# Performance work log

Hardware: AMD Instinct MI355X
Metric: run time of the kernel (lower is better)

The kernel has to match this reference:

```python
import jax, jax.numpy as jnp
import numpy as np

T, B, INP, HID = 256, 128, 512, 512
LAST_K, RSIZE = 32, 64
ATTN = 1.0
NEG = -1e30  # stands in for float('-inf') in the mask; softmax weight is exactly 0 either way


def setup_inputs() -> dict:
    key = jax.random.key(0)
    ks = jax.random.split(key, 6)
    xav = lambda fi, fo: (2.0 / (fi + fo)) ** 0.5
    x = jax.random.normal(ks[0], (T, B, INP), jnp.float32)
    # torch Linear weights stored transposed so y = x @ W (+ b)
    Uw = jax.random.normal(ks[1], (INP, HID), jnp.float32) * xav(INP, HID)
    Ub = jnp.zeros((HID,), jnp.float32)
    Vw = jax.random.normal(ks[2], (HID, HID), jnp.float32) * xav(HID, HID)
    Uaw = jax.random.normal(ks[3], (HID, HID), jnp.float32) * xav(HID, HID)
    Vaw = jax.random.normal(ks[4], (HID, HID), jnp.float32) * xav(HID, HID)
    v = jax.random.normal(ks[5], (HID,), jnp.float32) * xav(1, HID)
    return {"x": x, "Uw": Uw, "Ub": Ub, "Vw": Vw, "Uaw": Uaw, "Vaw": Vaw, "v": v}


def reference(x, Uw, Ub, Vw, Uaw, Vaw, v):
    Tlen, Bsz, _ = x.shape
    H = Uw.shape[1]
    bidx = jnp.arange(Bsz)

    def step(carry, inp):
        xt, t = inp
        st, buf, slot_time, long_mem, long_mask, long_scores, buck, fcnt, lids = carry

        def first(_):
            # hidden is None -> zeros, so V(hidden) == 0; st is the pre-nonlinearity h
            pre = xt @ Uw + Ub
            return pre, jnp.tanh(pre), long_scores

        def later(_):
            va_st = st @ Vaw                                  # [B,H]
            # short-term memory attention (buf slot p holds h_{slot_time[p]}, -1 = empty)
            es = jnp.einsum('kbh,h->kb', jnp.tanh(va_st[None] + buf @ Uaw), v)
            es = jnp.where(slot_time[:, None] >= 0, es, NEG)  # mask empty slots
            es_l = jnp.einsum('rbh,h->rb', jnp.tanh(va_st[None] + long_mem @ Uaw), v) + long_mask
            alphas = jax.nn.softmax(jnp.concatenate([es, es_l], axis=0), axis=0)  # [K+R,B]
            comb = jnp.concatenate([buf, long_mem], axis=0)   # [K+R,B,H]
            ct = jnp.einsum('mb,mbh->bh', alphas, comb)
            last_h = buf[(t - 1) % LAST_K]                    # memory[-1] == h_{t-1}
            st_new = 0.5 * (last_h + ct * ATTN)
            h = jnp.tanh(xt @ Uw + Ub + st_new @ Vw)
            # detached accumulation of attention mass per timestep (long_scores[time] += alpha)
            det = jax.lax.stop_gradient(alphas[:LAST_K])
            valid = slot_time >= 0
            ls = long_scores.at[jnp.where(valid, slot_time, 0)].add(
                jnp.where(valid[:, None], det, 0.0))
            return st_new, h, ls

        st, h, long_scores = jax.lax.cond(t == 0, first, later, None)

        # --- conditional bucket eviction: candidate is h_{t-LAST_K} (oldest in buf) ---
        evict_step = t >= LAST_K
        cand = buf[t % LAST_K]                                # slot about to be overwritten
        score_t = long_scores[jnp.maximum(t - LAST_K, 0)]     # [B]
        minp = jnp.argmin(buck, axis=1)                       # [B]
        not_full = fcnt < RSIZE
        replace = score_t > buck[bidx, minp]
        do = evict_step & (not_full | replace)
        pos = jnp.where(not_full, fcnt, minp)                 # [B]
        long_mem = long_mem.at[pos, bidx].set(jnp.where(do[:, None], cand, long_mem[pos, bidx]))
        long_mask = long_mask.at[pos, bidx].set(jnp.where(do, 0.0, long_mask[pos, bidx]))
        buck = buck.at[bidx, pos].set(jnp.where(do, score_t, buck[bidx, pos]))
        lids = lids.at[bidx, pos].set(jnp.where(do, (t - LAST_K).astype(jnp.float32), lids[bidx, pos]))
        fcnt = jnp.where(do & not_full, fcnt + 1, fcnt)

        # append h to short-term circular buffer
        buf = buf.at[t % LAST_K].set(h)
        slot_time = slot_time.at[t % LAST_K].set(t)

        return (st, buf, slot_time, long_mem, long_mask, long_scores, buck, fcnt, lids), h

    carry0 = (
        jnp.zeros((Bsz, H), jnp.float32),                 # st
        jnp.zeros((LAST_K, Bsz, H), jnp.float32),         # short-term memory buffer
        -jnp.ones((LAST_K,), jnp.int32),                  # time stored in each buf slot
        jnp.zeros((RSIZE, Bsz, H), jnp.float32),          # long_mem buckets
        jnp.full((RSIZE, Bsz), NEG, jnp.float32),         # long_mask
        jnp.zeros((Tlen, Bsz), jnp.float32),              # long_scores
        jnp.zeros((Bsz, RSIZE), jnp.float32),             # buck_scores
        jnp.zeros((Bsz,), jnp.int32),                     # bucket fill count
        -jnp.ones((Bsz, RSIZE), jnp.float32),             # long_ids
    )
    _, hs = jax.lax.scan(step, carry0, (x, jnp.arange(Tlen)))
    return hs  # [T,B,H] hidden state at every step
```

## Files before the change

### kernel.cpp

```cpp
#include <hip/hip_runtime.h>
#include <hip/hip_bf16.h>
#include <cstddef>

#define kT 256
#define kB 128
#define kINP 512
#define kH 512
#define kK 32
#define kR 64
#define kNEG (-1e30f)

__device__ __forceinline__ void ag_store(float* p, float v) {
    __hip_atomic_store(p, v, __ATOMIC_RELAXED, __HIP_MEMORY_SCOPE_AGENT);
}
__device__ __forceinline__ float ag_load(const float* p) {
    return __hip_atomic_load(p, __ATOMIC_RELAXED, __HIP_MEMORY_SCOPE_AGENT);
}

__device__ __forceinline__ float ftanh(float x)
{
    float e = __expf(2.0f * x);
    return 1.0f - 2.0f * __builtin_amdgcn_rcpf(e + 1.0f);
}

__global__ __launch_bounds__(256) void gemm_xu(
    const float* __restrict__ A, const float* __restrict__ W,
    const float* __restrict__ bias, float* __restrict__ C)
{
    __shared__ float At[32][68];
    __shared__ float Ws[32][68];
    const int tid = threadIdx.x;
    const int n0 = blockIdx.x * 64;
    const int m0 = blockIdx.y * 64;
    const int tx = tid & 15, ty = tid >> 4;
    const int arow = tid >> 3, ak = (tid & 7) << 2;
    const int wrow = tid >> 4, wc = (tid & 15) << 2;

    float acc[4][4] = {};

    for (int k0 = 0; k0 < kINP; k0 += 32) {
        float4 a0 = *reinterpret_cast<const float4*>(&A[(size_t)(m0 + arow) * kINP + k0 + ak]);
        float4 a1 = *reinterpret_cast<const float4*>(&A[(size_t)(m0 + 32 + arow) * kINP + k0 + ak]);
        float4 w0 = *reinterpret_cast<const float4*>(&W[(size_t)(k0 + wrow) * kH + n0 + wc]);
        float4 w1 = *reinterpret_cast<const float4*>(&W[(size_t)(k0 + wrow + 16) * kH + n0 + wc]);
        __syncthreads();
        At[ak + 0][arow] = a0.x; At[ak + 1][arow] = a0.y;
        At[ak + 2][arow] = a0.z; At[ak + 3][arow] = a0.w;
        At[ak + 0][32 + arow] = a1.x; At[ak + 1][32 + arow] = a1.y;
        At[ak + 2][32 + arow] = a1.z; At[ak + 3][32 + arow] = a1.w;
        *reinterpret_cast<float4*>(&Ws[wrow][wc]) = w0;
        *reinterpret_cast<float4*>(&Ws[wrow + 16][wc]) = w1;
        __syncthreads();
#pragma unroll
        for (int kk = 0; kk < 32; ++kk) {
            float4 a4 = *reinterpret_cast<float4*>(&At[kk][ty * 4]);
            float4 w4 = *reinterpret_cast<float4*>(&Ws[kk][tx * 4]);
            float a_[4] = {a4.x, a4.y, a4.z, a4.w};
            float w_[4] = {w4.x, w4.y, w4.z, w4.w};
#pragma unroll
            for (int r = 0; r < 4; ++r)
#pragma unroll
                for (int c = 0; c < 4; ++c)
                    acc[r][c] += a_[r] * w_[c];
        }
    }

#pragma unroll
    for (int r = 0; r < 4; ++r) {
        int m = m0 + ty * 4 + r;
#pragma unroll
        for (int c = 0; c < 4; ++c) {
            int n = n0 + tx * 4 + c;
            C[(size_t)m * kH + n] = acc[r][c] + bias[n];
        }
    }
}

__global__ __launch_bounds__(256) void init_flags_k(int* __restrict__ flags)
{
    int i = blockIdx.x * 256 + threadIdx.x;
    if (i < kB * 3 * 2) flags[i] = 0;
}

__global__ __launch_bounds__(1024) void rnn_pair(
    const float* __restrict__ Vw, const float* __restrict__ Vaw,
    const float* __restrict__ Uaw, const float* __restrict__ vvec,
    const float* __restrict__ XU, float* __restrict__ lngU,
    float* __restrict__ hs, float* __restrict__ esx,
    float* __restrict__ stx, int* __restrict__ flags)
{
    extern __shared__ float dyn[];
    float* shortH = dyn;
    float* shortU = dyn + 32 * 256;
    float* longH  = dyn + 64 * 256;
    float* part   = dyn + 128 * 256;
    const int PSTR = 264;

    const int bid = blockIdx.x;
    const int b = bid >> 1, half = bid & 1;
    const int C0 = half << 8;
    const int P0 = (half ^ 1) << 8;
    const int tid = threadIdx.x;
    const int kq = tid >> 6;
    const int lane = tid & 63;
    const int c4 = lane << 2;

    __shared__ __align__(16) float h_sh[512];
    __shared__ __align__(16) float st_sh[512];
    __shared__ __align__(16) float va_sh[256];
    __shared__ __align__(16) float v_sh[256];
    __shared__ float es_own[96], es_sh[96], w_sh[96];
    __shared__ int   rowm[96];
    __shared__ float lsc_sh[kT];
    __shared__ float buck_sh[kR];
    __shared__ int   lidx_sh[kR];
    __shared__ int   fcnt_sh, evict_pos;
    __shared__ float red0, red1;

    float* lngU_b = lngU + (size_t)bid * kR * 256;

    int* fC_own = &flags[(b * 3 + 0) * 2 + half];
    int* fB_own = &flags[(b * 3 + 1) * 2 + half];
    int* fS_own = &flags[(b * 3 + 2) * 2 + half];
    int* fC_par = &flags[(b * 3 + 0) * 2 + (half ^ 1)];
    int* fB_par = &flags[(b * 3 + 1) * 2 + (half ^ 1)];
    int* fS_par = &flags[(b * 3 + 2) * 2 + (half ^ 1)];

    auto wait_ge = [&](int* f, int target) {
        if (tid == 0) {
            while (__hip_atomic_load(f, __ATOMIC_RELAXED, __HIP_MEMORY_SCOPE_AGENT) < target)
                __builtin_amdgcn_s_sleep(1);
        }
        __syncthreads();
    };
    auto set_flag = [&](int* f, int val) {
        __syncthreads();
        if (tid == 0)
            __hip_atomic_store(f, val, __ATOMIC_RELAXED, __HIP_MEMORY_SCOPE_AGENT);
    };

    if (tid < 256) { v_sh[tid] = vvec[C0 + tid]; lsc_sh[tid] = 0.0f; }
    if (tid < kR) { buck_sh[tid] = 0.0f; lidx_sh[tid] = -1; }
    if (tid == 0) fcnt_sh = 0;
    if (tid < 512) st_sh[tid] = XU[(size_t)b * kH + tid];
    __syncthreads();
    if (tid < 256) {
        float h0 = tanhf(st_sh[C0 + tid]);
        h_sh[C0 + tid] = h0;
        shortH[tid] = h0;
        ag_store(&hs[(size_t)b * kH + C0 + tid], h0);
    }
    set_flag(fC_own, 1);
    {
        float4 acc = {0, 0, 0, 0};
#pragma unroll 8
        for (int k = kq; k < kH; k += 16) {
            float s = st_sh[k];
            const float4 w = *reinterpret_cast<const float4*>(&Vaw[(size_t)k * kH + C0 + c4]);
            acc.x += s * w.x; acc.y += s * w.y; acc.z += s * w.z; acc.w += s * w.w;
        }
        *reinterpret_cast<float4*>(&part[kq * PSTR + c4]) = acc;
        __syncthreads();
        if (tid < 256) {
            float s = 0.0f;
#pragma unroll
            for (int j = 0; j < 16; ++j) s += part[j * PSTR + tid];
            va_sh[tid] = s;
        }
        __syncthreads();
    }

    for (int t = 1; t < kT; ++t) {
        float xu_reg = 0.0f;
        if (tid < 256) xu_reg = XU[((size_t)t * kB + b) * kH + C0 + tid];

        float4 accA = {0, 0, 0, 0};
#pragma unroll 8
        for (int k = C0 + kq; k < C0 + 256; k += 16) {
            float s = h_sh[k];
            const float4 w = *reinterpret_cast<const float4*>(&Uaw[(size_t)k * kH + C0 + c4]);
            accA.x += s * w.x; accA.y += s * w.y; accA.z += s * w.z; accA.w += s * w.w;
        }
        if (tid < 96) {
            int row;
            if (tid < kK) { int md = (t + 31 - tid) & 31; row = t - 1 - md; }
            else row = lidx_sh[tid - kK];
            rowm[tid] = row;
        }
        wait_ge(fC_par, t);
        if (tid < 256) h_sh[P0 + tid] = ag_load(&hs[((size_t)(t - 1) * kB + b) * kH + P0 + tid]);
        __syncthreads();
#pragma unroll 8
        for (int k = P0 + kq; k < P0 + 256; k += 16) {
            float s = h_sh[k];
            const float4 w = *reinterpret_cast<const float4*>(&Uaw[(size_t)k * kH + C0 + c4]);
            accA.x += s * w.x; accA.y += s * w.y; accA.z += s * w.z; accA.w += s * w.w;
        }
        *reinterpret_cast<float4*>(&part[kq * PSTR + c4]) = accA;
        __syncthreads();
        if (tid < 256) {
            float u = 0.0f;
#pragma unroll
            for (int j = 0; j < 16; ++j) u += part[j * PSTR + tid];
            shortU[((t - 1) & 31) * 256 + tid] = u;
        }
        __syncthreads();

        {
            float4 uu[6];
            int rv[6];
#pragma unroll
            for (int r = 0; r < 6; ++r) {
                int m = kq + (r << 4);
                int row = rowm[m];
                rv[r] = row;
                uu[r] = make_float4(0.f, 0.f, 0.f, 0.f);
                if (row >= 0) {
                    const float* up = (m < kK) ? &shortU[m * 256]
                                               : &lngU_b[(size_t)(m - kK) * 256];
                    uu[r] = *reinterpret_cast<const float4*>(&up[c4]);
                }
            }
            const float4 vav = *reinterpret_cast<const float4*>(&va_sh[c4]);
            const float4 vvv = *reinterpret_cast<const float4*>(&v_sh[c4]);
#pragma unroll
            for (int r = 0; r < 6; ++r) {
                float p = 0.0f;
                if (rv[r] >= 0) {
                    p = vvv.x * ftanh(vav.x + uu[r].x) + vvv.y * ftanh(vav.y + uu[r].y)
                      + vvv.z * ftanh(vav.z + uu[r].z) + vvv.w * ftanh(vav.w + uu[r].w);
                }
#pragma unroll
                for (int off = 32; off; off >>= 1) p += __shfl_down(p, off);
                if (lane == 0) es_own[kq + (r << 4)] = p;
            }
        }
        __syncthreads();
        if (tid < 96) ag_store(&esx[((size_t)b * 2 + half) * 96 + tid], es_own[tid]);
        set_flag(fB_own, t);
        wait_ge(fB_par, t);
        if (tid < 96) {
            float e = kNEG;
            if (rowm[tid] >= 0)
                e = es_own[tid] + ag_load(&esx[((size_t)b * 2 + (half ^ 1)) * 96 + tid]);
            es_sh[tid] = e;
        }
        __syncthreads();

        if (tid < 64) {
            float a = es_sh[tid];
            float c = (tid < 32) ? es_sh[64 + tid] : kNEG;
            float mx = fmaxf(a, c);
#pragma unroll
            for (int off = 32; off; off >>= 1) mx = fmaxf(mx, __shfl_xor(mx, off));
            if (tid == 0) red0 = mx;
        }
        __syncthreads();
        if (tid < 96) w_sh[tid] = __expf(es_sh[tid] - red0);
        __syncthreads();
        if (tid < 64) {
            float a = w_sh[tid] + ((tid < 32) ? w_sh[64 + tid] : 0.0f);
#pragma unroll
            for (int off = 32; off; off >>= 1) a += __shfl_xor(a, off);
            if (tid == 0) red1 = 1.0f / a;
        }
        __syncthreads();

        {
            float4 hv[6]; float wq[6];
#pragma unroll
            for (int r = 0; r < 6; ++r) {
                int m = kq + (r << 4);
                int row = rowm[m];
                hv[r] = make_float4(0.f, 0.f, 0.f, 0.f); wq[r] = 0.0f;
                if (row >= 0) {
                    const float* hp = (m < kK) ? &shortH[m * 256]
                                               : &longH[(m - kK) * 256];
                    hv[r] = *reinterpret_cast<const float4*>(&hp[c4]);
                    wq[r] = w_sh[m];
                }
            }
            float4 acc = {0, 0, 0, 0};
#pragma unroll
            for (int r = 0; r < 6; ++r) {
                acc.x += wq[r] * hv[r].x; acc.y += wq[r] * hv[r].y;
                acc.z += wq[r] * hv[r].z; acc.w += wq[r] * hv[r].w;
            }
            *reinterpret_cast<float4*>(&part[kq * PSTR + c4]) = acc;
        }
        __syncthreads();
        if (tid < 256) {
            float ct = 0.0f;
#pragma unroll
            for (int j = 0; j < 16; ++j) ct += part[j * PSTR + tid];
            float stv = 0.5f * (h_sh[C0 + tid] + ct * red1);
            st_sh[C0 + tid] = stv;
            ag_store(&stx[(size_t)b * kH + C0 + tid], stv);
        }
        set_flag(fS_own, t);

        if (tid < kK) {
            int row = rowm[tid];
            if (row >= 0) lsc_sh[row] += w_sh[tid] * red1;
        }
        __syncthreads();
        if (tid == 0) {
            int ep = -1;
            if (t >= kK) {
                float score = lsc_sh[t - kK];
                int fc = fcnt_sh;
                bool nf = fc < kR;
                float mn = buck_sh[0]; int mp = 0;
                for (int r = 1; r < kR; ++r) {
                    float bv = buck_sh[r];
                    if (bv < mn) { mn = bv; mp = r; }
                }
                if (nf || score > mn) {
                    ep = nf ? fc : mp;
                    lidx_sh[ep] = t - kK;
                    buck_sh[ep] = score;
                    if (nf) fcnt_sh = fc + 1;
                }
            }
            evict_pos = ep;
        }
        __syncthreads();
        if (evict_pos >= 0 && tid < 256) {
            longH[evict_pos * 256 + tid] = shortH[(t & 31) * 256 + tid];
            lngU_b[(size_t)evict_pos * 256 + tid] = shortU[(t & 31) * 256 + tid];
        }

        {
            float4 aw = {0, 0, 0, 0};
#pragma unroll 8
            for (int k = C0 + kq; k < C0 + 256; k += 16) {
                float s = st_sh[k];
                const float4 w = *reinterpret_cast<const float4*>(&Vw[(size_t)k * kH + C0 + c4]);
                aw.x += s * w.x; aw.y += s * w.y; aw.z += s * w.z; aw.w += s * w.w;
            }
            wait_ge(fS_par, t);
            if (tid < 256) st_sh[P0 + tid] = ag_load(&stx[(size_t)b * kH + P0 + tid]);
            __syncthreads();
#pragma unroll 8
            for (int k = P0 + kq; k < P0 + 256; k += 16) {
                float s = st_sh[k];
                const float4 w = *reinterpret_cast<const float4*>(&Vw[(size_t)k * kH + C0 + c4]);
                aw.x += s * w.x; aw.y += s * w.y; aw.z += s * w.z; aw.w += s * w.w;
            }
            *reinterpret_cast<float4*>(&part[kq * PSTR + c4]) = aw;
        }
        __syncthreads();
        if (tid < 256) {
            float hpre = xu_reg;
#pragma unroll
            for (int j = 0; j < 16; ++j) hpre += part[j * PSTR + tid];
            float hv = tanhf(hpre);
            h_sh[C0 + tid] = hv;
            shortH[(t & 31) * 256 + tid] = hv;
            ag_store(&hs[((size_t)t * kB + b) * kH + C0 + tid], hv);
        }
        set_flag(fC_own, t + 1);

        {
            float4 av = {0, 0, 0, 0};
#pragma unroll 8
            for (int k = kq; k < kH; k += 16) {
                float s = st_sh[k];
                const float4 w = *reinterpret_cast<const float4*>(&Vaw[(size_t)k * kH + C0 + c4]);
                av.x += s * w.x; av.y += s * w.y; av.z += s * w.z; av.w += s * w.w;
            }
            *reinterpret_cast<float4*>(&part[kq * PSTR + c4]) = av;
        }
        __syncthreads();
        if (tid < 256) {
            float vn = 0.0f;
#pragma unroll
            for (int j = 0; j < 16; ++j) vn += part[j * PSTR + tid];
            va_sh[tid] = vn;
        }
        __syncthreads();
    }
}

extern "C" void kernel_launch(void* const* d_in, const int* in_sizes, int n_in,
                              void* d_out, int out_size, void* d_ws, size_t ws_size,
                              hipStream_t stream)
{
    const float* x   = (const float*)d_in[0];
    const float* Uw  = (const float*)d_in[1];
    const float* Ub  = (const float*)d_in[2];
    const float* Vw  = (const float*)d_in[3];
    const float* Uaw = (const float*)d_in[4];
    const float* Vaw = (const float*)d_in[5];
    const float* vv  = (const float*)d_in[6];
    float* hs = (float*)d_out;

    float* ws = (float*)d_ws;
    const size_t TBH = (size_t)kT * kB * kH;
    float* XU   = ws;
    float* lngU = XU + TBH;
    float* esx  = lngU + (size_t)2 * kB * kR * 256;
    float* stx  = esx + (size_t)kB * 2 * 96;
    int*   flags = (int*)(stx + (size_t)kB * kH);

    const int dyn_bytes = (32 * 256 + 32 * 256 + 64 * 256 + 16 * 264) * 4;
    hipFuncSetAttribute(reinterpret_cast<const void*>(rnn_pair),
                        hipFuncAttributeMaxDynamicSharedMemorySize, dyn_bytes);

    init_flags_k<<<3, 256, 0, stream>>>(flags);

    gemm_xu<<<dim3(kH / 64, (kT * kB) / 64), 256, 0, stream>>>(x, Uw, Ub, XU);

    rnn_pair<<<2 * kB, 1024, dyn_bytes, stream>>>(
        Vw, Vaw, Uaw, vv, XU, lngU, hs, esx, stx, flags);
}
```

Baseline: 5.658 ms.

## Overlap Vaw projection with Uaw matvec by splitting waves across both

Instead of computing st@Vaw as a separate phase at the end of each step (and once before the loop), half of the waves now compute it while the other half compute the own-half h@Uaw product. The remote-half Uaw product after the parity wait is handled by those same 8 waves only. Both reductions run in one pass, dropping two barriers per step and putting the Vaw work in the window before the cross-block flag wait. The risk is that the post-wait Uaw work now uses half as many waves, which lengthens that stage of the critical path.

```diff
diff --git a/kernel.cpp b/kernel.cpp
--- a/kernel.cpp
+++ b/kernel.cpp
@@ -102,6 +102,7 @@
     const int P0 = (half ^ 1) << 8;
     const int tid = threadIdx.x;
     const int kq = tid >> 6;
+    const int kq8 = kq & 7;
     const int lane = tid & 63;
     const int c4 = lane << 2;
 
@@ -151,35 +152,26 @@
         ag_store(&hs[(size_t)b * kH + C0 + tid], h0);
     }
     set_flag(fC_own, 1);
-    {
-        float4 acc = {0, 0, 0, 0};
-#pragma unroll 8
-        for (int k = kq; k < kH; k += 16) {
-            float s = st_sh[k];
-            const float4 w = *reinterpret_cast<const float4*>(&Vaw[(size_t)k * kH + C0 + c4]);
-            acc.x += s * w.x; acc.y += s * w.y; acc.z += s * w.z; acc.w += s * w.w;
-        }
-        *reinterpret_cast<float4*>(&part[kq * PSTR + c4]) = acc;
-        __syncthreads();
-        if (tid < 256) {
-            float s = 0.0f;
-#pragma unroll
-            for (int j = 0; j < 16; ++j) s += part[j * PSTR + tid];
-            va_sh[tid] = s;
-        }
-        __syncthreads();
-    }
 
     for (int t = 1; t < kT; ++t) {
         float xu_reg = 0.0f;
         if (tid < 256) xu_reg = XU[((size_t)t * kB + b) * kH + C0 + tid];
 
         float4 accA = {0, 0, 0, 0};
-#pragma unroll 8
-        for (int k = C0 + kq; k < C0 + 256; k += 16) {
-            float s = h_sh[k];
-            const float4 w = *reinterpret_cast<const float4*>(&Uaw[(size_t)k * kH + C0 + c4]);
-            accA.x += s * w.x; accA.y += s * w.y; accA.z += s * w.z; accA.w += s * w.w;
+        if (kq >= 8) {
+#pragma unroll 8
+            for (int k = kq8; k < kH; k += 8) {
+                float s = st_sh[k];
+                const float4 w = *reinterpret_cast<const float4*>(&Vaw[(size_t)k * kH + C0 + c4]);
+                accA.x += s * w.x; accA.y += s * w.y; accA.z += s * w.z; accA.w += s * w.w;
+            }
+        } else {
+#pragma unroll 8
+            for (int k = C0 + kq8; k < C0 + 256; k += 8) {
+                float s = h_sh[k];
+                const float4 w = *reinterpret_cast<const float4*>(&Uaw[(size_t)k * kH + C0 + c4]);
+                accA.x += s * w.x; accA.y += s * w.y; accA.z += s * w.z; accA.w += s * w.w;
+            }
         }
         if (tid < 96) {
             int row;
@@ -190,19 +182,28 @@
         wait_ge(fC_par, t);
         if (tid < 256) h_sh[P0 + tid] = ag_load(&hs[((size_t)(t - 1) * kB + b) * kH + P0 + tid]);
         __syncthreads();
-#pragma unroll 8
-        for (int k = P0 + kq; k < P0 + 256; k += 16) {
-            float s = h_sh[k];
-            const float4 w = *reinterpret_cast<const float4*>(&Uaw[(size_t)k * kH + C0 + c4]);
-            accA.x += s * w.x; accA.y += s * w.y; accA.z += s * w.z; accA.w += s * w.w;
+        if (kq < 8) {
+#pragma unroll 8
+            for (int k = P0 + kq8; k < P0 + 256; k += 8) {
+                float s = h_sh[k];
+                const float4 w = *reinterpret_cast<const float4*>(&Uaw[(size_t)k * kH + C0 + c4]);
+                accA.x += s * w.x; accA.y += s * w.y; accA.z += s * w.z; accA.w += s * w.w;
+            }
         }
         *reinterpret_cast<float4*>(&part[kq * PSTR + c4]) = accA;
         __syncthreads();
-        if (tid < 256) {
-            float u = 0.0f;
-#pragma unroll
-            for (int j = 0; j < 16; ++j) u += part[j * PSTR + tid];
-            shortU[((t - 1) & 31) * 256 + tid] = u;
+        if (tid < 512) {
+            int col = tid & 255;
+            float acc = 0.0f;
+            if (tid < 256) {
+#pragma unroll
+                for (int j = 0; j < 8; ++j) acc += part[j * PSTR + col];
+                shortU[((t - 1) & 31) * 256 + col] = acc;
+            } else {
+#pragma unroll
+                for (int j = 8; j < 16; ++j) acc += part[j * PSTR + col];
+                va_sh[col] = acc;
+            }
         }
         __syncthreads();
 
@@ -360,25 +361,6 @@
             ag_store(&hs[((size_t)t * kB + b) * kH + C0 + tid], hv);
         }
         set_flag(fC_own, t + 1);
-
-        {
-            float4 av = {0, 0, 0, 0};
-#pragma unroll 8
-            for (int k = kq; k < kH; k += 16) {
-                float s = st_sh[k];
-                const float4 w = *reinterpret_cast<const float4*>(&Vaw[(size_t)k * kH + C0 + c4]);
-                av.x += s * w.x; av.y += s * w.y; av.z += s * w.z; av.w += s * w.w;
-            }
-            *reinterpret_cast<float4*>(&part[kq * PSTR + c4]) = av;
-        }
-        __syncthreads();
-        if (tid < 256) {
-            float vn = 0.0f;
-#pragma unroll
-            for (int j = 0; j < 16; ++j) vn += part[j * PSTR + tid];
-            va_sh[tid] = vn;
-        }
-        __syncthreads();
     }
 }
 
```

Result: slower. 7.650 ms (+35.2%).

## Split recurrent kernel into quad blocks handling two batch rows per column quarter

Applied to the files above, without the earlier changes.

The per-step recurrence moves from a pair of blocks per batch row (each owning half the hidden columns) to groups of four blocks that each own a quarter of the columns for two batch rows. Each loaded weight float4 is reused across both batch rows, halving weight traffic per row, and each block's shared-memory footprint per row shrinks. In exchange, every step now needs four-way flag synchronization and gathers partial energies from three peers, which adds cross-block latency on the serial critical path. It also changes the lsc bookkeeping to a 64-entry ring that is reset after use.

```diff
diff --git a/kernel.cpp b/kernel.cpp
--- a/kernel.cpp
+++ b/kernel.cpp
@@ -79,10 +79,26 @@
 __global__ __launch_bounds__(256) void init_flags_k(int* __restrict__ flags)
 {
     int i = blockIdx.x * 256 + threadIdx.x;
-    if (i < kB * 3 * 2) flags[i] = 0;
-}
-
-__global__ __launch_bounds__(1024) void rnn_pair(
+    if (i < 64 * 3 * 4) flags[i] = 0;
+}
+
+#define MV_STEP(Wmat, xs, i, A0, A1) { \
+    int k_ = (i)*32 + (w << 1) + half32; \
+    const float4 wt_ = *reinterpret_cast<const float4*>(&Wmat[(size_t)k_ * kH + C0 + c4]); \
+    float s0_ = xs[0][k_], s1_ = xs[1][k_]; \
+    A0.x += s0_*wt_.x; A0.y += s0_*wt_.y; A0.z += s0_*wt_.z; A0.w += s0_*wt_.w; \
+    A1.x += s1_*wt_.x; A1.y += s1_*wt_.y; A1.z += s1_*wt_.z; A1.w += s1_*wt_.w; }
+
+#define MV_FINISH(A0, A1) { \
+    A0.x += __shfl_xor(A0.x, 32); A0.y += __shfl_xor(A0.y, 32); \
+    A0.z += __shfl_xor(A0.z, 32); A0.w += __shfl_xor(A0.w, 32); \
+    A1.x += __shfl_xor(A1.x, 32); A1.y += __shfl_xor(A1.y, 32); \
+    A1.z += __shfl_xor(A1.z, 32); A1.w += __shfl_xor(A1.w, 32); \
+    if (lane < 32) { \
+        *reinterpret_cast<float4*>(&part[(w*2 + 0)*128 + c4]) = A0; \
+        *reinterpret_cast<float4*>(&part[(w*2 + 1)*128 + c4]) = A1; } }
+
+__global__ __launch_bounds__(1024) void rnn_quad(
     const float* __restrict__ Vw, const float* __restrict__ Vaw,
     const float* __restrict__ Uaw, const float* __restrict__ vvec,
     const float* __restrict__ XU, float* __restrict__ lngU,
@@ -91,294 +107,304 @@
 {
     extern __shared__ float dyn[];
     float* shortH = dyn;
-    float* shortU = dyn + 32 * 256;
-    float* longH  = dyn + 64 * 256;
-    float* part   = dyn + 128 * 256;
-    const int PSTR = 264;
+    float* shortU = dyn + 8192;
+    float* longH  = dyn + 16384;
+    float* part   = dyn + 32768;
 
     const int bid = blockIdx.x;
-    const int b = bid >> 1, half = bid & 1;
-    const int C0 = half << 8;
-    const int P0 = (half ^ 1) << 8;
+    const int g = bid >> 2, q = bid & 3;
+    const int bA = g << 1;
+    const int C0 = q << 7;
     const int tid = threadIdx.x;
-    const int kq = tid >> 6;
+    const int w = tid >> 6;
     const int lane = tid & 63;
-    const int c4 = lane << 2;
-
-    __shared__ __align__(16) float h_sh[512];
-    __shared__ __align__(16) float st_sh[512];
-    __shared__ __align__(16) float va_sh[256];
-    __shared__ __align__(16) float v_sh[256];
-    __shared__ float es_own[96], es_sh[96], w_sh[96];
-    __shared__ int   rowm[96];
-    __shared__ float lsc_sh[kT];
-    __shared__ float buck_sh[kR];
-    __shared__ int   lidx_sh[kR];
-    __shared__ int   fcnt_sh, evict_pos;
-    __shared__ float red0, red1;
-
-    float* lngU_b = lngU + (size_t)bid * kR * 256;
-
-    int* fC_own = &flags[(b * 3 + 0) * 2 + half];
-    int* fB_own = &flags[(b * 3 + 1) * 2 + half];
-    int* fS_own = &flags[(b * 3 + 2) * 2 + half];
-    int* fC_par = &flags[(b * 3 + 0) * 2 + (half ^ 1)];
-    int* fB_par = &flags[(b * 3 + 1) * 2 + (half ^ 1)];
-    int* fS_par = &flags[(b * 3 + 2) * 2 + (half ^ 1)];
-
-    auto wait_ge = [&](int* f, int target) {
-        if (tid == 0) {
+    const int half32 = lane >> 5;
+    const int c4 = (lane & 31) << 2;
+    const int c2 = lane << 1;
+    const int i0 = q << 2;
+
+    __shared__ __align__(16) float h_sh[2][512];
+    __shared__ __align__(16) float st_sh[2][512];
+    __shared__ __align__(16) float va_sh[2][128];
+    __shared__ __align__(16) float v_sh[128];
+    __shared__ float es_own[2][96], es_sh[2][96], w_sh[2][96];
+    __shared__ int   rowm[2][96];
+    __shared__ float lsc_sh[2][64];
+    __shared__ float buck_sh[2][64];
+    __shared__ int   lidx_sh[2][64];
+    __shared__ int   fcnt_sh[2], evict_pos[2];
+    __shared__ float red0[2], red1[2];
+
+    float* lngU_b = lngU + (size_t)bid * 2 * kR * 128;
+    const int fbase = g * 12;
+
+    auto wait3 = [&](int phase, int target) {
+        if (tid < 3) {
+            int p = tid + (tid >= q ? 1 : 0);
+            int* f = &flags[fbase + phase * 4 + p];
             while (__hip_atomic_load(f, __ATOMIC_RELAXED, __HIP_MEMORY_SCOPE_AGENT) < target)
                 __builtin_amdgcn_s_sleep(1);
         }
         __syncthreads();
     };
-    auto set_flag = [&](int* f, int val) {
+    auto set_flag = [&](int phase, int val) {
         __syncthreads();
         if (tid == 0)
-            __hip_atomic_store(f, val, __ATOMIC_RELAXED, __HIP_MEMORY_SCOPE_AGENT);
+            __hip_atomic_store(&flags[fbase + phase * 4 + q], val,
+                               __ATOMIC_RELAXED, __HIP_MEMORY_SCOPE_AGENT);
     };
 
-    if (tid < 256) { v_sh[tid] = vvec[C0 + tid]; lsc_sh[tid] = 0.0f; }
-    if (tid < kR) { buck_sh[tid] = 0.0f; lidx_sh[tid] = -1; }
-    if (tid == 0) fcnt_sh = 0;
-    if (tid < 512) st_sh[tid] = XU[(size_t)b * kH + tid];
+    if (tid < 128) v_sh[tid] = vvec[C0 + tid];
+    if (tid < 128) {
+        int bb = tid >> 6, s = tid & 63;
+        lsc_sh[bb][s] = 0.0f; buck_sh[bb][s] = 0.0f; lidx_sh[bb][s] = -1;
+    }
+    if (tid < 2) fcnt_sh[tid] = 0;
+    {
+        int bb = tid >> 9, col = tid & 511;
+        st_sh[bb][col] = XU[(size_t)(bA + bb) * kH + col];
+    }
     __syncthreads();
     if (tid < 256) {
-        float h0 = tanhf(st_sh[C0 + tid]);
-        h_sh[C0 + tid] = h0;
-        shortH[tid] = h0;
-        ag_store(&hs[(size_t)b * kH + C0 + tid], h0);
-    }
-    set_flag(fC_own, 1);
+        int bb = tid >> 7, col = tid & 127;
+        float h0 = tanhf(st_sh[bb][C0 + col]);
+        h_sh[bb][C0 + col] = h0;
+        shortH[(bb * 32 + 0) * 128 + col] = h0;
+        ag_store(&hs[(size_t)(bA + bb) * kH + C0 + col], h0);
+    }
+    set_flag(0, 1);
     {
-        float4 acc = {0, 0, 0, 0};
-#pragma unroll 8
-        for (int k = kq; k < kH; k += 16) {
-            float s = st_sh[k];
-            const float4 w = *reinterpret_cast<const float4*>(&Vaw[(size_t)k * kH + C0 + c4]);
-            acc.x += s * w.x; acc.y += s * w.y; acc.z += s * w.z; acc.w += s * w.w;
-        }
-        *reinterpret_cast<float4*>(&part[kq * PSTR + c4]) = acc;
+        float4 a0 = {0,0,0,0}, a1 = {0,0,0,0};
+#pragma unroll
+        for (int i = 0; i < 16; ++i) MV_STEP(Vaw, st_sh, i, a0, a1);
+        MV_FINISH(a0, a1);
         __syncthreads();
         if (tid < 256) {
+            int bb = tid >> 7, col = tid & 127;
             float s = 0.0f;
 #pragma unroll
-            for (int j = 0; j < 16; ++j) s += part[j * PSTR + tid];
-            va_sh[tid] = s;
+            for (int j = 0; j < 16; ++j) s += part[(j * 2 + bb) * 128 + col];
+            va_sh[bb][col] = s;
         }
         __syncthreads();
     }
 
     for (int t = 1; t < kT; ++t) {
         float xu_reg = 0.0f;
-        if (tid < 256) xu_reg = XU[((size_t)t * kB + b) * kH + C0 + tid];
-
-        float4 accA = {0, 0, 0, 0};
-#pragma unroll 8
-        for (int k = C0 + kq; k < C0 + 256; k += 16) {
-            float s = h_sh[k];
-            const float4 w = *reinterpret_cast<const float4*>(&Uaw[(size_t)k * kH + C0 + c4]);
-            accA.x += s * w.x; accA.y += s * w.y; accA.z += s * w.z; accA.w += s * w.w;
-        }
-        if (tid < 96) {
+        if (tid < 256) {
+            int bb = tid >> 7, col = tid & 127;
+            xu_reg = XU[((size_t)t * kB + (bA + bb)) * kH + C0 + col];
+        }
+
+        float4 aU0 = {0,0,0,0}, aU1 = {0,0,0,0};
+#pragma unroll
+        for (int i = 0; i < 4; ++i) MV_STEP(Uaw, h_sh, i0 + i, aU0, aU1);
+        if (tid < 192) {
+            int bb = (tid >= 96), m = tid - bb * 96;
             int row;
-            if (tid < kK) { int md = (t + 31 - tid) & 31; row = t - 1 - md; }
-            else row = lidx_sh[tid - kK];
-            rowm[tid] = row;
-        }
-        wait_ge(fC_par, t);
-        if (tid < 256) h_sh[P0 + tid] = ag_load(&hs[((size_t)(t - 1) * kB + b) * kH + P0 + tid]);
-        __syncthreads();
-#pragma unroll 8
-        for (int k = P0 + kq; k < P0 + 256; k += 16) {
-            float s = h_sh[k];
-            const float4 w = *reinterpret_cast<const float4*>(&Uaw[(size_t)k * kH + C0 + c4]);
-            accA.x += s * w.x; accA.y += s * w.y; accA.z += s * w.z; accA.w += s * w.w;
-        }
-        *reinterpret_cast<float4*>(&part[kq * PSTR + c4]) = accA;
+            if (m < kK) { int md = (t + 31 - m) & 31; row = t - 1 - md; }
+            else row = lidx_sh[bb][m - kK];
+            rowm[bb][m] = row;
+        }
+        wait3(0, t);
+        if (tid < 768) {
+            int bb = tid / 384, j = tid - bb * 384;
+            int pq = j >> 7, col = j & 127;
+            int qq = pq + (pq >= q ? 1 : 0);
+            h_sh[bb][qq * 128 + col] =
+                ag_load(&hs[((size_t)(t - 1) * kB + (bA + bb)) * kH + qq * 128 + col]);
+        }
+        __syncthreads();
+        for (int i = 0; i < i0; ++i) MV_STEP(Uaw, h_sh, i, aU0, aU1);
+        for (int i = i0 + 4; i < 16; ++i) MV_STEP(Uaw, h_sh, i, aU0, aU1);
+        MV_FINISH(aU0, aU1);
         __syncthreads();
         if (tid < 256) {
+            int bb = tid >> 7, col = tid & 127;
             float u = 0.0f;
 #pragma unroll
-            for (int j = 0; j < 16; ++j) u += part[j * PSTR + tid];
-            shortU[((t - 1) & 31) * 256 + tid] = u;
+            for (int j = 0; j < 16; ++j) u += part[(j * 2 + bb) * 128 + col];
+            shortU[(bb * 32 + ((t - 1) & 31)) * 128 + col] = u;
         }
         __syncthreads();
 
         {
-            float4 uu[6];
-            int rv[6];
-#pragma unroll
-            for (int r = 0; r < 6; ++r) {
-                int m = kq + (r << 4);
-                int row = rowm[m];
-                rv[r] = row;
-                uu[r] = make_float4(0.f, 0.f, 0.f, 0.f);
+            int bb = w >> 3, wr = w & 7;
+            float2 vav = *reinterpret_cast<const float2*>(&va_sh[bb][c2]);
+            float2 vvv = *reinterpret_cast<const float2*>(&v_sh[c2]);
+#pragma unroll
+            for (int r = 0; r < 12; ++r) {
+                int m = wr + (r << 3);
+                int row = rowm[bb][m];
+                float p = 0.0f;
                 if (row >= 0) {
-                    const float* up = (m < kK) ? &shortU[m * 256]
-                                               : &lngU_b[(size_t)(m - kK) * 256];
-                    uu[r] = *reinterpret_cast<const float4*>(&up[c4]);
+                    const float* up = (m < kK) ? &shortU[(bb * 32 + m) * 128]
+                                               : &lngU_b[(size_t)(bb * kR + (m - kK)) * 128];
+                    float2 uu = *reinterpret_cast<const float2*>(&up[c2]);
+                    p = vvv.x * ftanh(vav.x + uu.x) + vvv.y * ftanh(vav.y + uu.y);
                 }
-            }
-            const float4 vav = *reinterpret_cast<const float4*>(&va_sh[c4]);
-            const float4 vvv = *reinterpret_cast<const float4*>(&v_sh[c4]);
-#pragma unroll
-            for (int r = 0; r < 6; ++r) {
-                float p = 0.0f;
-                if (rv[r] >= 0) {
-                    p = vvv.x * ftanh(vav.x + uu[r].x) + vvv.y * ftanh(vav.y + uu[r].y)
-                      + vvv.z * ftanh(vav.z + uu[r].z) + vvv.w * ftanh(vav.w + uu[r].w);
+#pragma unroll
+                for (int off = 32; off; off >>= 1) p += __shfl_down(p, off);
+                if (lane == 0) es_own[bb][m] = p;
+            }
+        }
+        __syncthreads();
+        if (tid < 192) {
+            int bb = (tid >= 96), m = tid - bb * 96;
+            ag_store(&esx[(size_t)bid * 192 + bb * 96 + m], es_own[bb][m]);
+        }
+        set_flag(1, t);
+        wait3(1, t);
+        if (tid < 192) {
+            int bb = (tid >= 96), m = tid - bb * 96;
+            float e = kNEG;
+            if (rowm[bb][m] >= 0) {
+                e = 0.0f;
+#pragma unroll
+                for (int p = 0; p < 4; ++p)
+                    e += ag_load(&esx[(size_t)(g * 4 + p) * 192 + bb * 96 + m]);
+            }
+            es_sh[bb][m] = e;
+        }
+        __syncthreads();
+
+        if (w < 2) {
+            float a = es_sh[w][lane];
+            float b2 = (lane < 32) ? es_sh[w][64 + lane] : kNEG;
+            float mx = fmaxf(a, b2);
+#pragma unroll
+            for (int off = 32; off; off >>= 1) mx = fmaxf(mx, __shfl_xor(mx, off));
+            if (lane == 0) red0[w] = mx;
+        }
+        __syncthreads();
+        if (tid < 192) {
+            int bb = (tid >= 96), m = tid - bb * 96;
+            w_sh[bb][m] = __expf(es_sh[bb][m] - red0[bb]);
+        }
+        __syncthreads();
+        if (w < 2) {
+            float a = w_sh[w][lane] + ((lane < 32) ? w_sh[w][64 + lane] : 0.0f);
+#pragma unroll
+            for (int off = 32; off; off >>= 1) a += __shfl_xor(a, off);
+            if (lane == 0) red1[w] = 1.0f / a;
+        }
+        __syncthreads();
+
+        {
+            int bb = w >> 3, wr = w & 7;
+            float2 acc = {0.0f, 0.0f};
+#pragma unroll
+            for (int r = 0; r < 12; ++r) {
+                int m = wr + (r << 3);
+                int row = rowm[bb][m];
+                if (row >= 0) {
+                    const float* hp = (m < kK) ? &shortH[(bb * 32 + m) * 128]
+                                               : &longH[(bb * kR + (m - kK)) * 128];
+                    float2 hv = *reinterpret_cast<const float2*>(&hp[c2]);
+                    float wq = w_sh[bb][m];
+                    acc.x += wq * hv.x; acc.y += wq * hv.y;
                 }
-#pragma unroll
-                for (int off = 32; off; off >>= 1) p += __shfl_down(p, off);
-                if (lane == 0) es_own[kq + (r << 4)] = p;
-            }
-        }
-        __syncthreads();
-        if (tid < 96) ag_store(&esx[((size_t)b * 2 + half) * 96 + tid], es_own[tid]);
-        set_flag(fB_own, t);
-        wait_ge(fB_par, t);
-        if (tid < 96) {
-            float e = kNEG;
-            if (rowm[tid] >= 0)
-                e = es_own[tid] + ag_load(&esx[((size_t)b * 2 + (half ^ 1)) * 96 + tid]);
-            es_sh[tid] = e;
-        }
-        __syncthreads();
+            }
+            *reinterpret_cast<float2*>(&part[w * 128 + c2]) = acc;
+        }
+        __syncthreads();
+        if (tid < 256) {
+            int bb = tid >> 7, col = tid & 127;
+            float ct = 0.0f;
+#pragma unroll
+            for (int j = 0; j < 8; ++j) ct += part[(bb * 8 + j) * 128 + col];
+            float stv = 0.5f * (h_sh[bb][C0 + col] + ct * red1[bb]);
+            st_sh[bb][C0 + col] = stv;
+            ag_store(&stx[(size_t)(bA + bb) * kH + C0 + col], stv);
+        }
+        set_flag(2, t);
 
         if (tid < 64) {
-            float a = es_sh[tid];
-            float c = (tid < 32) ? es_sh[64 + tid] : kNEG;
-            float mx = fmaxf(a, c);
-#pragma unroll
-            for (int off = 32; off; off >>= 1) mx = fmaxf(mx, __shfl_xor(mx, off));
-            if (tid == 0) red0 = mx;
-        }
-        __syncthreads();
-        if (tid < 96) w_sh[tid] = __expf(es_sh[tid] - red0);
-        __syncthreads();
-        if (tid < 64) {
-            float a = w_sh[tid] + ((tid < 32) ? w_sh[64 + tid] : 0.0f);
-#pragma unroll
-            for (int off = 32; off; off >>= 1) a += __shfl_xor(a, off);
-            if (tid == 0) red1 = 1.0f / a;
-        }
-        __syncthreads();
-
-        {
-            float4 hv[6]; float wq[6];
-#pragma unroll
-            for (int r = 0; r < 6; ++r) {
-                int m = kq + (r << 4);
-                int row = rowm[m];
-                hv[r] = make_float4(0.f, 0.f, 0.f, 0.f); wq[r] = 0.0f;
-                if (row >= 0) {
-                    const float* hp = (m < kK) ? &shortH[m * 256]
-                                               : &longH[(m - kK) * 256];
-                    hv[r] = *reinterpret_cast<const float4*>(&hp[c4]);
-                    wq[r] = w_sh[m];
-                }
-            }
-            float4 acc = {0, 0, 0, 0};
-#pragma unroll
-            for (int r = 0; r < 6; ++r) {
-                acc.x += wq[r] * hv[r].x; acc.y += wq[r] * hv[r].y;
-                acc.z += wq[r] * hv[r].z; acc.w += wq[r] * hv[r].w;
-            }
-            *reinterpret_cast<float4*>(&part[kq * PSTR + c4]) = acc;
-        }
-        __syncthreads();
-        if (tid < 256) {
-            float ct = 0.0f;
-#pragma unroll
-            for (int j = 0; j < 16; ++j) ct += part[j * PSTR + tid];
-            float stv = 0.5f * (h_sh[C0 + tid] + ct * red1);
-            st_sh[C0 + tid] = stv;
-            ag_store(&stx[(size_t)b * kH + C0 + tid], stv);
-        }
-        set_flag(fS_own, t);
-
-        if (tid < kK) {
-            int row = rowm[tid];
-            if (row >= 0) lsc_sh[row] += w_sh[tid] * red1;
-        }
-        __syncthreads();
-        if (tid == 0) {
-            int ep = -1;
+            int bb = tid >> 5, s = tid & 31;
+            int row = rowm[bb][s];
+            if (row >= 0) lsc_sh[bb][row & 63] += w_sh[bb][s] * red1[bb];
+        }
+        __syncthreads();
+        if (tid < 2) {
+            int bb = tid, ep = -1;
             if (t >= kK) {
-                float score = lsc_sh[t - kK];
-                int fc = fcnt_sh;
+                float score = lsc_sh[bb][(t - kK) & 63];
+                lsc_sh[bb][(t - kK) & 63] = 0.0f;
+                int fc = fcnt_sh[bb];
                 bool nf = fc < kR;
-                float mn = buck_sh[0]; int mp = 0;
-                for (int r = 1; r < kR; ++r) {
-                    float bv = buck_sh[r];
-                    if (bv < mn) { mn = bv; mp = r; }
+                float mn = buck_sh[bb][0]; int mp = 0;
+                for (int r2 = 1; r2 < kR; ++r2) {
+                    float bv = buck_sh[bb][r2];
+                    if (bv < mn) { mn = bv; mp = r2; }
                 }
                 if (nf || score > mn) {
                     ep = nf ? fc : mp;
-                    lidx_sh[ep] = t - kK;
-                    buck_sh[ep] = score;
-                    if (nf) fcnt_sh = fc + 1;
+                    lidx_sh[bb][ep] = t - kK;
+                    buck_sh[bb][ep] = score;
+                    if (nf) fcnt_sh[bb] = fc + 1;
                 }
             }
-            evict_pos = ep;
-        }
-        __syncthreads();
-        if (evict_pos >= 0 && tid < 256) {
-            longH[evict_pos * 256 + tid] = shortH[(t & 31) * 256 + tid];
-            lngU_b[(size_t)evict_pos * 256 + tid] = shortU[(t & 31) * 256 + tid];
-        }
+            evict_pos[bb] = ep;
+        }
+        __syncthreads();
+        if (tid < 512) {
+            int bb = tid >> 8, j = tid & 255;
+            int ep = evict_pos[bb];
+            if (ep >= 0) {
+                int slot = t & 31;
+                if (j < 128)
+                    longH[(bb * kR + ep) * 128 + j] = shortH[(bb * 32 + slot) * 128 + j];
+                else {
+                    int col = j - 128;
+                    lngU_b[(size_t)(bb * kR + ep) * 128 + col] =
+                        shortU[(bb * 32 + slot) * 128 + col];
+                }
+            }
+        }
+
+        float4 aW0 = {0,0,0,0}, aW1 = {0,0,0,0};
+#pragma unroll
+        for (int i = 0; i < 4; ++i) MV_STEP(Vw, st_sh, i0 + i, aW0, aW1);
+        wait3(2, t);
+        if (tid < 768) {
+            int bb = tid / 384, j = tid - bb * 384;
+            int pq = j >> 7, col = j & 127;
+            int qq = pq + (pq >= q ? 1 : 0);
+            st_sh[bb][qq * 128 + col] =
+                ag_load(&stx[(size_t)(bA + bb) * kH + qq * 128 + col]);
+        }
+        __syncthreads();
+        for (int i = 0; i < i0; ++i) MV_STEP(Vw, st_sh, i, aW0, aW1);
+        for (int i = i0 + 4; i < 16; ++i) MV_STEP(Vw, st_sh, i, aW0, aW1);
+        MV_FINISH(aW0, aW1);
+        __syncthreads();
+        if (tid < 256) {
+            int bb = tid >> 7, col = tid & 127;
+            float hpre = xu_reg;
+#pragma unroll
+            for (int j = 0; j < 16; ++j) hpre += part[(j * 2 + bb) * 128 + col];
+            float hv = tanhf(hpre);
+            h_sh[bb][C0 + col] = hv;
+            shortH[(bb * 32 + (t & 31)) * 128 + col] = hv;
+            ag_store(&hs[((size_t)t * kB + (bA + bb)) * kH + C0 + col], hv);
+        }
+        set_flag(0, t + 1);
 
         {
-            float4 aw = {0, 0, 0, 0};
-#pragma unroll 8
-            for (int k = C0 + kq; k < C0 + 256; k += 16) {
-                float s = st_sh[k];
-                const float4 w = *reinterpret_cast<const float4*>(&Vw[(size_t)k * kH + C0 + c4]);
-                aw.x += s * w.x; aw.y += s * w.y; aw.z += s * w.z; aw.w += s * w.w;
-            }
-            wait_ge(fS_par, t);
-            if (tid < 256) st_sh[P0 + tid] = ag_load(&stx[(size_t)b * kH + P0 + tid]);
+            float4 aV0 = {0,0,0,0}, aV1 = {0,0,0,0};
+#pragma unroll
+            for (int i = 0; i < 16; ++i) MV_STEP(Vaw, st_sh, i, aV0, aV1);
+            MV_FINISH(aV0, aV1);
             __syncthreads();
-#pragma unroll 8
-            for (int k = P0 + kq; k < P0 + 256; k += 16) {
-                float s = st_sh[k];
-                const float4 w = *reinterpret_cast<const float4*>(&Vw[(size_t)k * kH + C0 + c4]);
-                aw.x += s * w.x; aw.y += s * w.y; aw.z += s * w.z; aw.w += s * w.w;
-            }
-            *reinterpret_cast<float4*>(&part[kq * PSTR + c4]) = aw;
-        }
-        __syncthreads();
-        if (tid < 256) {
-            float hpre = xu_reg;
-#pragma unroll
-            for (int j = 0; j < 16; ++j) hpre += part[j * PSTR + tid];
-            float hv = tanhf(hpre);
-            h_sh[C0 + tid] = hv;
-            shortH[(t & 31) * 256 + tid] = hv;
-            ag_store(&hs[((size_t)t * kB + b) * kH + C0 + tid], hv);
-        }
-        set_flag(fC_own, t + 1);
-
-        {
-            float4 av = {0, 0, 0, 0};
-#pragma unroll 8
-            for (int k = kq; k < kH; k += 16) {
-                float s = st_sh[k];
-                const float4 w = *reinterpret_cast<const float4*>(&Vaw[(size_t)k * kH + C0 + c4]);
-                av.x += s * w.x; av.y += s * w.y; av.z += s * w.z; av.w += s * w.w;
-            }
-            *reinterpret_cast<float4*>(&part[kq * PSTR + c4]) = av;
-        }
-        __syncthreads();
-        if (tid < 256) {
-            float vn = 0.0f;
-#pragma unroll
-            for (int j = 0; j < 16; ++j) vn += part[j * PSTR + tid];
-            va_sh[tid] = vn;
-        }
-        __syncthreads();
+            if (tid < 256) {
+                int bb = tid >> 7, col = tid & 127;
+                float s = 0.0f;
+#pragma unroll
+                for (int j = 0; j < 16; ++j) s += part[(j * 2 + bb) * 128 + col];
+                va_sh[bb][col] = s;
+            }
+            __syncthreads();
+        }
     }
 }
 
@@ -399,18 +425,18 @@
     const size_t TBH = (size_t)kT * kB * kH;
     float* XU   = ws;
     float* lngU = XU + TBH;
-    float* esx  = lngU + (size_t)2 * kB * kR * 256;
-    float* stx  = esx + (size_t)kB * 2 * 96;
+    float* esx  = lngU + (size_t)256 * 2 * kR * 128;
+    float* stx  = esx + (size_t)256 * 192;
     int*   flags = (int*)(stx + (size_t)kB * kH);
 
-    const int dyn_bytes = (32 * 256 + 32 * 256 + 64 * 256 + 16 * 264) * 4;
-    hipFuncSetAttribute(reinterpret_cast<const void*>(rnn_pair),
+    const int dyn_bytes = (8192 + 8192 + 16384 + 4096) * 4;
+    hipFuncSetAttribute(reinterpret_cast<const void*>(rnn_quad),
                         hipFuncAttributeMaxDynamicSharedMemorySize, dyn_bytes);
 
     init_flags_k<<<3, 256, 0, stream>>>(flags);
 
     gemm_xu<<<dim3(kH / 64, (kT * kB) / 64), 256, 0, stream>>>(x, Uw, Ub, XU);
 
-    rnn_pair<<<2 * kB, 1024, dyn_bytes, stream>>>(
+    rnn_quad<<<256, 1024, dyn_bytes, stream>>>(
         Vw, Vaw, Uaw, vv, XU, lngU, hs, esx, stx, flags);
 }
```

Measured after the change: 14.46 ms. +155.5%, slower.
